# Kernel optimization log

Hardware: AMD Instinct MI355X
Metric: run time of the kernel (lower is better)

The kernel has to match this reference:

```python
import jax, jax.numpy as jnp
import numpy as np


def setup_inputs() -> dict:
    key = jax.random.key(0)
    k1, k2, k3, k4, k5 = jax.random.split(key, 5)
    B, S, E2, D = 32, 2048, 1024, 512
    return {
        "output_encoder": jax.random.normal(k1, (B, S, E2), dtype=jnp.float32),
        "last_hidden_decoder": jax.random.normal(k2, (B, D), dtype=jnp.float32),
        "W_att": jax.random.normal(k3, (E2 + D, D), dtype=jnp.float32) * 0.02,
        "b_att": jax.random.normal(k4, (D,), dtype=jnp.float32) * 0.02,
        "v": jax.random.normal(k5, (D,), dtype=jnp.float32) * 0.02,
    }


def reference(output_encoder, last_hidden_decoder, W_att, b_att, v):
    # output_encoder: (B, S, E2); last_hidden_decoder: (B, D)
    B, S, E2 = output_encoder.shape
    D = last_hidden_decoder.shape[-1]
    # Split W_att to avoid materializing the repeated+concat tensor:
    # concat(enc, dec) @ W == enc @ W_enc + dec @ W_dec  (dec broadcast over seq)
    W_enc, W_dec = W_att[:E2], W_att[E2:]
    dec_proj = last_hidden_decoder @ W_dec  # (B, D)
    energy = jnp.tanh(jnp.einsum("bse,ed->bsd", output_encoder, W_enc)
                      + dec_proj[:, None, :] + b_att)  # (B, S, D)
    attention = jnp.einsum("bsd,d->bs", energy, v)  # (B, S)
    attention_weights = jax.nn.softmax(attention, axis=1)  # (B, S)
    # context: (B, 1, E2)
    context = jnp.einsum("bs,bse->be", attention_weights, output_encoder)[:, None, :]
    return context
```

## Files before the change

### kernel.cpp

```cpp
#include <hip/hip_runtime.h>
#include <stdint.h>


typedef __attribute__((ext_vector_type(8))) __bf16 bf16x8;
typedef __attribute__((ext_vector_type(4))) float f32x4;

__device__ __forceinline__ uint16_t f32_to_bf16_rne(float f) {
  union { float f; uint32_t u; } v; v.f = f;
  uint32_t u = v.u;
  return (uint16_t)((u + 0x7FFFu + ((u >> 16) & 1u)) >> 16);
}

__device__ __forceinline__ float tanh_fast(float x) {
  float e = __expf(2.0f * x);
  return 1.0f - 2.0f * __builtin_amdgcn_rcpf(e + 1.0f);
}

__global__ __launch_bounds__(256) void prep_kernel(
    const float* __restrict__ dec,
    const float* __restrict__ Watt,
    const float* __restrict__ batt,
    float* __restrict__ att,
    float* __restrict__ cbias,
    uint16_t* __restrict__ Wb,
    float* __restrict__ out)
{
  const int t = blockIdx.x * 256 + threadIdx.x;

  for (int i = t; i < 65536; i += 16384) att[i] = 0.0f;
  for (int i = t; i < 32768; i += 16384) out[i] = 0.0f;

  {
    const int b = t >> 9, d = t & 511;
    const float* wd = Watt + 1024 * 512 + d;
    const float* dv = dec + b * 512;
    float s0 = 0.f, s1 = 0.f, s2 = 0.f, s3 = 0.f;
    #pragma unroll 4
    for (int k = 0; k < 512; k += 4) {
      s0 += dv[k + 0] * wd[(k + 0) * 512];
      s1 += dv[k + 1] * wd[(k + 1) * 512];
      s2 += dv[k + 2] * wd[(k + 2) * 512];
      s3 += dv[k + 3] * wd[(k + 3) * 512];
    }
    cbias[t] = batt[d] + ((s0 + s1) + (s2 + s3));
  }

  uint4* WbV = (uint4*)Wb;
  #pragma unroll
  for (int i = 0; i < 4; ++i) {
    const int u = t + 16384 * i;
    const int d = u & 511;
    const int j = (u >> 9) & 7;
    const int c = u >> 12;
    uint32_t h[8];
    #pragma unroll
    for (int kk = 0; kk < 8; ++kk) {
      float f = Watt[(size_t)(c * 64 + j * 8 + kk) * 512 + d];
      h[kk] = f32_to_bf16_rne(f);
    }
    uint4 val;
    val.x = h[0] | (h[1] << 16);
    val.y = h[2] | (h[3] << 16);
    val.z = h[4] | (h[5] << 16);
    val.w = h[6] | (h[7] << 16);
    const int unit = (d * 128 + ((j * 16) ^ ((d & 7) << 4))) >> 4;
    WbV[c * 4096 + unit] = val;
  }
}

__global__ __launch_bounds__(256, 2) void energy_kernel(
    const float* __restrict__ x,
    const uint16_t* __restrict__ Wb,
    const float* __restrict__ cbias,
    const float* __restrict__ vvec,
    float* __restrict__ att)
{
  __shared__ __align__(16) uint8_t Albs[64 * 128];
  __shared__ __align__(16) uint8_t Blbs[512 * 128];

  const int tid  = threadIdx.x;
  const int lane = tid & 63;
  const int wave = tid >> 6;
  const int l15  = lane & 15;
  const int l4   = lane >> 4;
  const int brow0 = blockIdx.x * 64;
  const int b     = brow0 >> 11;

  f32x4 acc[4][8];
  #pragma unroll
  for (int mf = 0; mf < 4; ++mf)
    #pragma unroll
    for (int nf = 0; nf < 8; ++nf)
      acc[mf][nf] = (f32x4){0.f, 0.f, 0.f, 0.f};

  for (int c = 0; c < 16; ++c) {
    #pragma unroll
    for (int i = 0; i < 4; ++i) {
      const int idx = tid + 256 * i;
      const int r = idx >> 4, q = idx & 15;
      const float4 xv = *(const float4*)(x + (size_t)(brow0 + r) * 1024 + (size_t)(c * 64 + q * 4));
      uint32_t lo = (uint32_t)f32_to_bf16_rne(xv.x) | ((uint32_t)f32_to_bf16_rne(xv.y) << 16);
      uint32_t hi = (uint32_t)f32_to_bf16_rne(xv.z) | ((uint32_t)f32_to_bf16_rne(xv.w) << 16);
      const int off = r * 128 + ((q * 8) ^ ((r & 7) << 4));
      *(uint2*)(&Albs[off]) = make_uint2(lo, hi);
    }
    {
      const uint4* src = (const uint4*)Wb + (size_t)c * 4096;
      uint4* dst = (uint4*)Blbs;
      #pragma unroll
      for (int i = 0; i < 16; ++i) {
        const int u = tid + 256 * i;
        dst[u] = src[u];
      }
    }
    __syncthreads();

    #pragma unroll
    for (int ks = 0; ks < 2; ++ks) {
      bf16x8 af[4], bfr[8];
      #pragma unroll
      for (int mf = 0; mf < 4; ++mf) {
        const int r = l15 + 16 * mf;
        const int off = r * 128 + ((ks * 64 + l4 * 16) ^ ((r & 7) << 4));
        af[mf] = *(const bf16x8*)(&Albs[off]);
      }
      #pragma unroll
      for (int nf = 0; nf < 8; ++nf) {
        const int d = wave * 128 + nf * 16 + l15;
        const int off = d * 128 + ((ks * 64 + l4 * 16) ^ ((d & 7) << 4));
        bfr[nf] = *(const bf16x8*)(&Blbs[off]);
      }
      #pragma unroll
      for (int mf = 0; mf < 4; ++mf)
        #pragma unroll
        for (int nf = 0; nf < 8; ++nf)
          acc[mf][nf] = __builtin_amdgcn_mfma_f32_16x16x32_bf16(af[mf], bfr[nf], acc[mf][nf], 0, 0, 0);
    }
    __syncthreads();
  }

  float cb[8], vv[8];
  #pragma unroll
  for (int nf = 0; nf < 8; ++nf) {
    const int d = wave * 128 + nf * 16 + l15;
    cb[nf] = cbias[b * 512 + d];
    vv[nf] = vvec[d];
  }
  #pragma unroll
  for (int mf = 0; mf < 4; ++mf) {
    float s[4] = {0.f, 0.f, 0.f, 0.f};
    #pragma unroll
    for (int nf = 0; nf < 8; ++nf) {
      #pragma unroll
      for (int j = 0; j < 4; ++j) {
        const float e = acc[mf][nf][j] + cb[nf];
        s[j] += tanh_fast(e) * vv[nf];
      }
    }
    #pragma unroll
    for (int j = 0; j < 4; ++j) {
      float r = s[j];
      r += __shfl_xor(r, 1);
      r += __shfl_xor(r, 2);
      r += __shfl_xor(r, 4);
      r += __shfl_xor(r, 8);
      if (l15 == 0) atomicAdd(&att[brow0 + 16 * mf + 4 * l4 + j], r);
    }
  }
}

__global__ __launch_bounds__(256) void softmax_kernel(float* __restrict__ att) {
  const int b = blockIdx.x;
  float* row = att + b * 2048;
  const int tid = threadIdx.x;
  __shared__ float redm[4], reds[4];

  float vals[8];
  float m = -1e30f;
  #pragma unroll
  for (int i = 0; i < 8; ++i) { vals[i] = row[tid + 256 * i]; m = fmaxf(m, vals[i]); }
  #pragma unroll
  for (int msk = 1; msk < 64; msk <<= 1) m = fmaxf(m, __shfl_xor(m, msk));
  if ((tid & 63) == 0) redm[tid >> 6] = m;
  __syncthreads();
  m = fmaxf(fmaxf(redm[0], redm[1]), fmaxf(redm[2], redm[3]));

  float s = 0.f;
  #pragma unroll
  for (int i = 0; i < 8; ++i) { vals[i] = __expf(vals[i] - m); s += vals[i]; }
  #pragma unroll
  for (int msk = 1; msk < 64; msk <<= 1) s += __shfl_xor(s, msk);
  if ((tid & 63) == 0) reds[tid >> 6] = s;
  __syncthreads();
  const float inv = 1.0f / (((reds[0] + reds[1]) + (reds[2] + reds[3])));
  #pragma unroll
  for (int i = 0; i < 8; ++i) row[tid + 256 * i] = vals[i] * inv;
}

__global__ __launch_bounds__(256) void context_kernel(
    const float* __restrict__ x,
    const float* __restrict__ w,
    float* __restrict__ out)
{
  const int blk = blockIdx.x;
  const int b = blk >> 4, sc = blk & 15;
  const int tid = threadIdx.x;
  const float* xb = x + ((size_t)(b * 2048 + sc * 128)) * 1024 + tid * 4;
  const float* wb = w + b * 2048 + sc * 128;

  float4 acc = {0.f, 0.f, 0.f, 0.f};
  for (int si = 0; si < 128; ++si) {
    const float ww = wb[si];
    const float4 xv = *(const float4*)(xb + (size_t)si * 1024);
    acc.x += ww * xv.x;
    acc.y += ww * xv.y;
    acc.z += ww * xv.z;
    acc.w += ww * xv.w;
  }
  float* o = out + b * 1024 + tid * 4;
  atomicAdd(o + 0, acc.x);
  atomicAdd(o + 1, acc.y);
  atomicAdd(o + 2, acc.z);
  atomicAdd(o + 3, acc.w);
}

extern "C" void kernel_launch(void* const* d_in, const int* in_sizes, int n_in,
                              void* d_out, int out_size, void* d_ws, size_t ws_size,
                              hipStream_t stream) {
  const float* x    = (const float*)d_in[0];
  const float* dec  = (const float*)d_in[1];
  const float* Watt = (const float*)d_in[2];
  const float* batt = (const float*)d_in[3];
  const float* v    = (const float*)d_in[4];
  float* out = (float*)d_out;

  uint8_t* ws = (uint8_t*)d_ws;
  float*    att   = (float*)ws;
  float*    cbias = (float*)(ws + 256 * 1024);
  uint16_t* Wb    = (uint16_t*)(ws + 320 * 1024);

  prep_kernel<<<64, 256, 0, stream>>>(dec, Watt, batt, att, cbias, Wb, out);
  energy_kernel<<<1024, 256, 0, stream>>>(x, Wb, cbias, v, att);
  softmax_kernel<<<32, 256, 0, stream>>>(att);
  context_kernel<<<512, 256, 0, stream>>>(x, att, out);
}
```

Baseline: 160.7 us.

## Double-buffer energy GEMM with async LDS loads and 128-row tiles

The energy kernel now uses 512-thread blocks covering 128 rows, with 8 waves in a 2x4 grid, so each block reuses the bf16 weight chunk for twice as many rows. Weight chunks are copied straight into LDS with global_load_lds into double buffers. The next x chunk is prefetched into registers while the current chunk is computed, which removes one barrier per iteration. The aim is to hide load latency behind the MFMA work and to cut repeated weight traffic from L2. In exchange the block uses about 160KB of LDS, so only one block fits per CU and occupancy drops.

```diff
diff --git a/kernel.cpp b/kernel.cpp
--- a/kernel.cpp
+++ b/kernel.cpp
@@ -68,23 +68,36 @@
   }
 }
 
-__global__ __launch_bounds__(256, 2) void energy_kernel(
+__global__ __launch_bounds__(512, 2) void energy_kernel(
     const float* __restrict__ x,
     const uint16_t* __restrict__ Wb,
     const float* __restrict__ cbias,
     const float* __restrict__ vvec,
     float* __restrict__ att)
 {
-  __shared__ __align__(16) uint8_t Albs[64 * 128];
-  __shared__ __align__(16) uint8_t Blbs[512 * 128];
+  __shared__ __align__(16) uint8_t AL[2][128 * 128];
+  __shared__ __align__(16) uint8_t BL[2][512 * 128];
 
   const int tid  = threadIdx.x;
   const int lane = tid & 63;
   const int wave = tid >> 6;
+  const int wm   = wave >> 2;
+  const int wn   = wave & 3;
   const int l15  = lane & 15;
   const int l4   = lane >> 4;
-  const int brow0 = blockIdx.x * 64;
+  const int brow0 = blockIdx.x * 128;
   const int b     = brow0 >> 11;
+
+  int aoff[4];
+  const float* asrc[4];
+  #pragma unroll
+  for (int i = 0; i < 4; ++i) {
+    const int idx = tid + 512 * i;
+    const int r = idx >> 4, q = idx & 15;
+    aoff[i] = r * 128 + ((q * 8) ^ ((r & 7) << 4));
+    asrc[i] = x + (size_t)(brow0 + r) * 1024 + q * 4;
+  }
+  const uint8_t* wbase = (const uint8_t*)Wb + (lane << 4);
 
   f32x4 acc[4][8];
   #pragma unroll
@@ -93,42 +106,58 @@
     for (int nf = 0; nf < 8; ++nf)
       acc[mf][nf] = (f32x4){0.f, 0.f, 0.f, 0.f};
 
+  float4 av[4];
+  #pragma unroll
+  for (int i = 0; i < 4; ++i) av[i] = *(const float4*)(asrc[i]);
+  #pragma unroll
+  for (int i = 0; i < 8; ++i) {
+    const int u = i * 8 + wave;
+    __builtin_amdgcn_global_load_lds(
+        (const __attribute__((address_space(1))) uint32_t*)(wbase + u * 1024),
+        (__attribute__((address_space(3))) uint32_t*)(&BL[0][u * 1024]),
+        16, 0, 0);
+  }
+
   for (int c = 0; c < 16; ++c) {
+    uint8_t* Ab = AL[c & 1];
+    uint8_t* Bb = BL[c & 1];
+
     #pragma unroll
     for (int i = 0; i < 4; ++i) {
-      const int idx = tid + 256 * i;
-      const int r = idx >> 4, q = idx & 15;
-      const float4 xv = *(const float4*)(x + (size_t)(brow0 + r) * 1024 + (size_t)(c * 64 + q * 4));
-      uint32_t lo = (uint32_t)f32_to_bf16_rne(xv.x) | ((uint32_t)f32_to_bf16_rne(xv.y) << 16);
-      uint32_t hi = (uint32_t)f32_to_bf16_rne(xv.z) | ((uint32_t)f32_to_bf16_rne(xv.w) << 16);
-      const int off = r * 128 + ((q * 8) ^ ((r & 7) << 4));
-      *(uint2*)(&Albs[off]) = make_uint2(lo, hi);
-    }
-    {
-      const uint4* src = (const uint4*)Wb + (size_t)c * 4096;
-      uint4* dst = (uint4*)Blbs;
-      #pragma unroll
-      for (int i = 0; i < 16; ++i) {
-        const int u = tid + 256 * i;
-        dst[u] = src[u];
-      }
-    }
+      uint32_t lo = (uint32_t)f32_to_bf16_rne(av[i].x) | ((uint32_t)f32_to_bf16_rne(av[i].y) << 16);
+      uint32_t hi = (uint32_t)f32_to_bf16_rne(av[i].z) | ((uint32_t)f32_to_bf16_rne(av[i].w) << 16);
+      *(uint2*)(Ab + aoff[i]) = make_uint2(lo, hi);
+    }
+
     __syncthreads();
+
+    if (c < 15) {
+      const uint8_t* wc = wbase + ((size_t)(c + 1) << 16);
+      uint8_t* Bn = BL[(c + 1) & 1];
+      #pragma unroll
+      for (int i = 0; i < 8; ++i) {
+        const int u = i * 8 + wave;
+        __builtin_amdgcn_global_load_lds(
+            (const __attribute__((address_space(1))) uint32_t*)(wc + u * 1024),
+            (__attribute__((address_space(3))) uint32_t*)(Bn + u * 1024),
+            16, 0, 0);
+      }
+      #pragma unroll
+      for (int i = 0; i < 4; ++i) av[i] = *(const float4*)(asrc[i] + (c + 1) * 64);
+    }
 
     #pragma unroll
     for (int ks = 0; ks < 2; ++ks) {
       bf16x8 af[4], bfr[8];
       #pragma unroll
       for (int mf = 0; mf < 4; ++mf) {
-        const int r = l15 + 16 * mf;
-        const int off = r * 128 + ((ks * 64 + l4 * 16) ^ ((r & 7) << 4));
-        af[mf] = *(const bf16x8*)(&Albs[off]);
+        const int r = wm * 64 + mf * 16 + l15;
+        af[mf] = *(const bf16x8*)(Ab + r * 128 + ((ks * 64 + l4 * 16) ^ ((r & 7) << 4)));
       }
       #pragma unroll
       for (int nf = 0; nf < 8; ++nf) {
-        const int d = wave * 128 + nf * 16 + l15;
-        const int off = d * 128 + ((ks * 64 + l4 * 16) ^ ((d & 7) << 4));
-        bfr[nf] = *(const bf16x8*)(&Blbs[off]);
+        const int d = wn * 128 + nf * 16 + l15;
+        bfr[nf] = *(const bf16x8*)(Bb + d * 128 + ((ks * 64 + l4 * 16) ^ ((d & 7) << 4)));
       }
       #pragma unroll
       for (int mf = 0; mf < 4; ++mf)
@@ -136,13 +165,12 @@
         for (int nf = 0; nf < 8; ++nf)
           acc[mf][nf] = __builtin_amdgcn_mfma_f32_16x16x32_bf16(af[mf], bfr[nf], acc[mf][nf], 0, 0, 0);
     }
-    __syncthreads();
   }
 
   float cb[8], vv[8];
   #pragma unroll
   for (int nf = 0; nf < 8; ++nf) {
-    const int d = wave * 128 + nf * 16 + l15;
+    const int d = wn * 128 + nf * 16 + l15;
     cb[nf] = cbias[b * 512 + d];
     vv[nf] = vvec[d];
   }
@@ -164,7 +192,7 @@
       r += __shfl_xor(r, 2);
       r += __shfl_xor(r, 4);
       r += __shfl_xor(r, 8);
-      if (l15 == 0) atomicAdd(&att[brow0 + 16 * mf + 4 * l4 + j], r);
+      if (l15 == 0) atomicAdd(&att[brow0 + wm * 64 + mf * 16 + 4 * l4 + j], r);
     }
   }
 }
@@ -240,7 +268,7 @@
   uint16_t* Wb    = (uint16_t*)(ws + 320 * 1024);
 
   prep_kernel<<<64, 256, 0, stream>>>(dec, Watt, batt, att, cbias, Wb, out);
-  energy_kernel<<<1024, 256, 0, stream>>>(x, Wb, cbias, v, att);
+  energy_kernel<<<512, 512, 0, stream>>>(x, Wb, cbias, v, att);
   softmax_kernel<<<32, 256, 0, stream>>>(att);
   context_kernel<<<512, 256, 0, stream>>>(x, att, out);
 }
```

Result: no change. 162.9 us (+1.4%).
